# Performance work log

Hardware: AMD Instinct MI355X
Metric: run time of the kernel (lower is better)

## Reference

```python
import jax, jax.numpy as jnp
import numpy as np
from jax import lax

B, T, IN, H = 128, 1024, 256, 256


def setup_inputs() -> dict:
    key = jax.random.key(0)
    k1, k2, k3, k4 = jax.random.split(key, 4)
    return {
        "fullx": jax.random.normal(k1, (B, T, IN), dtype=jnp.float32),
        "h": jnp.zeros((B, H), dtype=jnp.float32),
        "c": jnp.zeros((B, H), dtype=jnp.float32),
        "wx": jax.random.normal(k2, (IN, 4 * H), dtype=jnp.float32) / (IN ** 0.5),
        "wh": jax.random.normal(k3, (H, 4 * H), dtype=jnp.float32) / (H ** 0.5),
        "b": jax.random.uniform(k4, (1, 4 * H), dtype=jnp.float32),
    }


def reference(fullx, h, c, wx, wh, b):
    hnum = h.shape[1]

    def step(carry, x_t):
        h, c = carry
        t = x_t @ wx + h @ wh + b  # [B, 4H]
        gate = jax.nn.sigmoid(t[:, : 3 * hnum])
        f = gate[:, :hnum]
        i = gate[:, hnum : 2 * hnum]
        o = gate[:, 2 * hnum : 3 * hnum]
        g = jnp.tanh(t[:, 3 * hnum : 4 * hnum])
        c_new = c * f + g * i
        h_new = jnp.tanh(c_new) * o
        return (h_new, c_new), h_new

    xs = jnp.swapaxes(fullx, 0, 1)  # [T, B, IN]
    (h_f, c_f), hs = lax.scan(step, (h, c), xs)
    fullh = jnp.swapaxes(hs, 0, 1)  # [B, T, H]
    return (fullh, h_f, c_f)
```

## Files before the change

kernel.cpp:

```cpp
#include <hip/hip_runtime.h>
#include <hip/hip_fp16.h>
#include <stdint.h>

#define Tdim 1024
#define INdim 256
#define Hdim 256
#define COLS 1024
#define NSLICE 8
#define NGRP 8
#define GB 16
#define UPB 32
#define CPB 128
#define NTHREADS 512
#define FLAG_STRIDE ((Tdim + 1) * NSLICE)
#define FLAG_BYTES (NGRP * FLAG_STRIDE * 4)
#define HBUF_OFF 266240

typedef _Float16 half8 __attribute__((ext_vector_type(8)));
typedef float f32x4 __attribute__((ext_vector_type(4)));

__device__ __forceinline__ uint16_t f2h(float f) {
    __half h = __float2half(f);
    return *reinterpret_cast<uint16_t*>(&h);
}
__device__ __forceinline__ float sigm(float v) {
    return __builtin_amdgcn_rcpf(1.f + __expf(-v));
}
__device__ __forceinline__ float tanhfast(float v) {
    float e = __expf(2.f * v);
    return 1.f - 2.f * __builtin_amdgcn_rcpf(e + 1.f);
}
__device__ __forceinline__ size_t hb_idx(int par, int grp, int m, int u) {
    return ((((size_t)par * NGRP + grp) * GB + m) << 8) | (size_t)u;
}

__global__ __launch_bounds__(NTHREADS, 1) void lstm_main(
    const float* __restrict__ x, const float* __restrict__ h0,
    const float* __restrict__ c0, const float* __restrict__ wx,
    const float* __restrict__ wh, const float* __restrict__ bias,
    float* __restrict__ out, uint32_t* flags, uint16_t* hbuf)
{
    const int tid   = threadIdx.x;
    const int grp   = blockIdx.x & 7;
    const int slice = blockIdx.x >> 3;
    const int lane  = tid & 63;
    const int wave  = tid >> 6;
    const int cw    = lane & 15;
    const int lhi   = lane >> 4;
    const int cl    = wave * 16 + cw;
    const int g     = cl & 3;
    const int ul    = cl >> 2;
    const int u     = slice * UPB + ul;
    const int gcol  = g * Hdim + u;

    __shared__ __align__(16) uint16_t Wl[CPB * 512];
    __shared__ __align__(16) uint16_t X[2][32][GB][8];
    __shared__ __align__(16) uint16_t Hs[32][GB][8];
    __shared__ __align__(16) uint16_t Hp16[GB][UPB];
    __shared__ __align__(16) float    Hpf[GB][UPB];

    for (int idx = tid; idx < CPB * 512; idx += NTHREADS) {
        int k  = idx >> 7;
        int ci = idx & 127;
        int uu = ci & 31, gg = ci >> 5;
        int cg = gg * Hdim + slice * UPB + uu;
        int c  = (uu << 2) | gg;
        float w = (k < INdim) ? wx[(size_t)k * COLS + cg]
                              : wh[(size_t)(k - INdim) * COLS + cg];
        int e = c * 512 + ((((k >> 3) ^ (c & 7)) << 3) | (k & 7));
        Wl[e] = f2h(w);
    }
    const int m_s  = tid >> 5;
    const int ko_s = tid & 31;
    {
        const float4* xs = reinterpret_cast<const float4*>(
            &x[((size_t)(grp * GB + m_s) * Tdim + 0) * INdim + ko_s * 8]);
        float4 a = xs[0], b = xs[1];
        uint16_t* xd = &X[0][ko_s][m_s][0];
        xd[0]=f2h(a.x); xd[1]=f2h(a.y); xd[2]=f2h(a.z); xd[3]=f2h(a.w);
        xd[4]=f2h(b.x); xd[5]=f2h(b.y); xd[6]=f2h(b.z); xd[7]=f2h(b.w);
    }
    float4 xp0, xp1;
    {
        const float4* xs = reinterpret_cast<const float4*>(
            &x[((size_t)(grp * GB + m_s) * Tdim + 1) * INdim + ko_s * 8]);
        xp0 = xs[0]; xp1 = xs[1];
    }
    if (tid < 64) {
        int m = tid >> 2, uo = tid & 3;
        int u0 = slice * UPB + uo * 8;
        const float4* hs = reinterpret_cast<const float4*>(
            &h0[(size_t)(grp * GB + m) * Hdim + u0]);
        float4 a = hs[0], b = hs[1];
        unsigned long long p0, p1;
        uint16_t* q0 = reinterpret_cast<uint16_t*>(&p0);
        uint16_t* q1 = reinterpret_cast<uint16_t*>(&p1);
        q0[0]=f2h(a.x); q0[1]=f2h(a.y); q0[2]=f2h(a.z); q0[3]=f2h(a.w);
        q1[0]=f2h(b.x); q1[1]=f2h(b.y); q1[2]=f2h(b.z); q1[3]=f2h(b.w);
        unsigned long long* hp =
            reinterpret_cast<unsigned long long*>(&hbuf[hb_idx(0, grp, m, u0)]);
        __hip_atomic_store(&hp[0], p0, __ATOMIC_RELAXED, __HIP_MEMORY_SCOPE_AGENT);
        __hip_atomic_store(&hp[1], p1, __ATOMIC_RELAXED, __HIP_MEMORY_SCOPE_AGENT);
    }
    float c_reg[4];
    #pragma unroll
    for (int r = 0; r < 4; ++r)
        c_reg[r] = c0[(size_t)(grp * GB + lhi * 4 + r) * Hdim + u];
    const float bv = bias[gcol];
    __syncthreads();
    uint32_t* fl = flags + grp * FLAG_STRIDE;
    if (tid == 0)
        __hip_atomic_store(&fl[slice], 1u, __ATOMIC_RELAXED, __HIP_MEMORY_SCOPE_AGENT);

    const uint32_t swz = (uint32_t)(cl & 7);
    const uint16_t* wrow = &Wl[cl * 512];
    float hv[4] = {0.f, 0.f, 0.f, 0.f};

    for (int t = 0; t < Tdim; ++t) {
        const int par = t & 1, pn = par ^ 1;

        {
            uint16_t* xd = &X[pn][ko_s][m_s][0];
            xd[0]=f2h(xp0.x); xd[1]=f2h(xp0.y); xd[2]=f2h(xp0.z); xd[3]=f2h(xp0.w);
            xd[4]=f2h(xp1.x); xd[5]=f2h(xp1.y); xd[6]=f2h(xp1.z); xd[7]=f2h(xp1.w);
        }
        {
            int tn = (t + 2 < Tdim) ? t + 2 : Tdim - 1;
            const float4* xs = reinterpret_cast<const float4*>(
                &x[((size_t)(grp * GB + m_s) * Tdim + tn) * INdim + ko_s * 8]);
            xp0 = xs[0]; xp1 = xs[1];
        }

        f32x4 acc0 = {0.f, 0.f, 0.f, 0.f}, acc1 = {0.f, 0.f, 0.f, 0.f};
        #pragma unroll
        for (int s = 0; s < 8; s += 2) {
            int ko0 = s * 4 + lhi, ko1 = ko0 + 4;
            half8 a0 = *reinterpret_cast<const half8*>(&X[par][ko0][cw][0]);
            half8 b0 = *reinterpret_cast<const half8*>(&wrow[(ko0 ^ swz) << 3]);
            acc0 = __builtin_amdgcn_mfma_f32_16x16x32_f16(a0, b0, acc0, 0, 0, 0);
            half8 a1 = *reinterpret_cast<const half8*>(&X[par][ko1][cw][0]);
            half8 b1 = *reinterpret_cast<const half8*>(&wrow[(ko1 ^ swz) << 3]);
            acc1 = __builtin_amdgcn_mfma_f32_16x16x32_f16(a1, b1, acc1, 0, 0, 0);
        }

        if (tid < NSLICE) {
            while (__hip_atomic_load(&fl[t * NSLICE + tid], __ATOMIC_RELAXED,
                                     __HIP_MEMORY_SCOPE_AGENT) == 0) {}
        }
        __syncthreads();

        {
            const unsigned long long* hp = reinterpret_cast<const unsigned long long*>(
                &hbuf[hb_idx(par, grp, m_s, ko_s * 8)]);
            unsigned long long h0v = __hip_atomic_load(&hp[0], __ATOMIC_RELAXED,
                                                       __HIP_MEMORY_SCOPE_AGENT);
            unsigned long long h1v = __hip_atomic_load(&hp[1], __ATOMIC_RELAXED,
                                                       __HIP_MEMORY_SCOPE_AGENT);
            *reinterpret_cast<unsigned long long*>(&Hs[ko_s][m_s][0]) = h0v;
            *reinterpret_cast<unsigned long long*>(&Hs[ko_s][m_s][4]) = h1v;
        }
        __syncthreads();

        #pragma unroll
        for (int s = 0; s < 8; s += 2) {
            int ko0 = s * 4 + lhi, ko1 = ko0 + 4;
            half8 a0 = *reinterpret_cast<const half8*>(&Hs[ko0][cw][0]);
            half8 b0 = *reinterpret_cast<const half8*>(&wrow[((32 + ko0) ^ swz) << 3]);
            acc0 = __builtin_amdgcn_mfma_f32_16x16x32_f16(a0, b0, acc0, 0, 0, 0);
            half8 a1 = *reinterpret_cast<const half8*>(&Hs[ko1][cw][0]);
            half8 b1 = *reinterpret_cast<const half8*>(&wrow[((32 + ko1) ^ swz) << 3]);
            acc1 = __builtin_amdgcn_mfma_f32_16x16x32_f16(a1, b1, acc1, 0, 0, 0);
        }

        #pragma unroll
        for (int r = 0; r < 4; ++r) {
            float tval = acc0[r] + acc1[r] + bv;
            float act = (g == 3) ? tanhfast(tval) : sigm(tval);
            float x1  = __shfl_xor(act, 1);
            float e0  = (g & 1) ? x1 : act;
            float o1  = (g & 1) ? act : x1;
            float e0s = __shfl_xor(e0, 2);
            float o1s = __shfl_xor(o1, 2);
            float f_ = (g < 2) ? e0  : e0s;
            float i_ = (g < 2) ? o1  : o1s;
            float o_ = (g < 2) ? e0s : e0;
            float g_ = (g < 2) ? o1s : o1;
            c_reg[r] = fmaf(c_reg[r], f_, g_ * i_);
            hv[r] = tanhfast(c_reg[r]) * o_;
        }

        if (g == 0) {
            #pragma unroll
            for (int r = 0; r < 4; ++r) {
                int m = lhi * 4 + r;
                Hp16[m][ul] = f2h(hv[r]);
                Hpf[m][ul]  = hv[r];
            }
        }
        __syncthreads();

        if (tid < 128) {
            int m = tid >> 3, q = tid & 7;
            unsigned long long v =
                *reinterpret_cast<const unsigned long long*>(&Hp16[m][q * 4]);
            __hip_atomic_store(reinterpret_cast<unsigned long long*>(
                                   &hbuf[hb_idx(pn, grp, m, slice * UPB + q * 4)]),
                               v, __ATOMIC_RELAXED, __HIP_MEMORY_SCOPE_AGENT);
        }
        __syncthreads();
        if (tid == 0)
            __hip_atomic_store(&fl[(t + 1) * NSLICE + slice], 1u,
                               __ATOMIC_RELAXED, __HIP_MEMORY_SCOPE_AGENT);

        if (tid >= 128 && tid < 256) {
            int j = tid - 128;
            int m = j >> 3, q = j & 7;
            float4 v = *reinterpret_cast<const float4*>(&Hpf[m][q * 4]);
            *reinterpret_cast<float4*>(
                &out[((size_t)(grp * GB + m) * Tdim + t) * Hdim + slice * UPB + q * 4]) = v;
        }
    }

    if (g == 0) {
        const size_t fsz = (size_t)(NGRP * GB) * Tdim * Hdim;
        #pragma unroll
        for (int r = 0; r < 4; ++r) {
            int m = lhi * 4 + r;
            out[fsz + (size_t)(grp * GB + m) * Hdim + u] = hv[r];
            out[fsz + (size_t)(NGRP * GB) * Hdim + (size_t)(grp * GB + m) * Hdim + u] = c_reg[r];
        }
    }
}

extern "C" void kernel_launch(void* const* d_in, const int* in_sizes, int n_in,
                              void* d_out, int out_size, void* d_ws, size_t ws_size,
                              hipStream_t stream) {
    const float* x    = (const float*)d_in[0];
    const float* h0   = (const float*)d_in[1];
    const float* c0   = (const float*)d_in[2];
    const float* wx   = (const float*)d_in[3];
    const float* wh   = (const float*)d_in[4];
    const float* bias = (const float*)d_in[5];
    float* out = (float*)d_out;
    uint32_t* flags = (uint32_t*)d_ws;
    uint16_t* hbuf  = (uint16_t*)((char*)d_ws + HBUF_OFF);

    hipMemsetAsync(flags, 0, FLAG_BYTES, stream);

    void* args[] = {(void*)&x, (void*)&h0, (void*)&c0, (void*)&wx, (void*)&wh,
                    (void*)&bias, (void*)&out, (void*)&flags, (void*)&hbuf};
    hipLaunchCooperativeKernel((const void*)lstm_main, dim3(NSLICE * NGRP),
                               dim3(NTHREADS), args, 0, stream);
}
```

Before: 2.601 ms.

## Keep weight fragments in registers and swizzle X/H shared layout

Each lane now loads its 16 weight fragments from LDS into registers once before the time loop, so the per-step MFMAs no longer read weights from shared memory. The X and H staging buffers are reordered to [m][k] with an XOR swizzle, which is meant to avoid bank conflicts. Stores into them are packed into single 16-byte writes instead of scalar half stores. This adds 64 VGPRs per lane to hold the weights, which is allowed since the kernel runs one 512-thread block per CU.

```diff
diff --git a/kernel.cpp b/kernel.cpp
--- a/kernel.cpp
+++ b/kernel.cpp
@@ -22,6 +22,9 @@
 __device__ __forceinline__ uint16_t f2h(float f) {
     __half h = __float2half(f);
     return *reinterpret_cast<uint16_t*>(&h);
+}
+__device__ __forceinline__ uint32_t pk2(float lo, float hi) {
+    return (uint32_t)f2h(lo) | ((uint32_t)f2h(hi) << 16);
 }
 __device__ __forceinline__ float sigm(float v) {
     return __builtin_amdgcn_rcpf(1.f + __expf(-v));
@@ -54,8 +57,8 @@
     const int gcol  = g * Hdim + u;
 
     __shared__ __align__(16) uint16_t Wl[CPB * 512];
-    __shared__ __align__(16) uint16_t X[2][32][GB][8];
-    __shared__ __align__(16) uint16_t Hs[32][GB][8];
+    __shared__ __align__(16) uint16_t X[2][GB][32][8];
+    __shared__ __align__(16) uint16_t Hs[GB][32][8];
     __shared__ __align__(16) uint16_t Hp16[GB][UPB];
     __shared__ __align__(16) float    Hpf[GB][UPB];
 
@@ -70,15 +73,15 @@
         int e = c * 512 + ((((k >> 3) ^ (c & 7)) << 3) | (k & 7));
         Wl[e] = f2h(w);
     }
-    const int m_s  = tid >> 5;
-    const int ko_s = tid & 31;
+    const int m_s   = tid >> 5;
+    const int ko_s  = tid & 31;
+    const int slt_s = ko_s ^ (m_s & 7);
     {
         const float4* xs = reinterpret_cast<const float4*>(
             &x[((size_t)(grp * GB + m_s) * Tdim + 0) * INdim + ko_s * 8]);
         float4 a = xs[0], b = xs[1];
-        uint16_t* xd = &X[0][ko_s][m_s][0];
-        xd[0]=f2h(a.x); xd[1]=f2h(a.y); xd[2]=f2h(a.z); xd[3]=f2h(a.w);
-        xd[4]=f2h(b.x); xd[5]=f2h(b.y); xd[6]=f2h(b.z); xd[7]=f2h(b.w);
+        uint4 pkv = {pk2(a.x, a.y), pk2(a.z, a.w), pk2(b.x, b.y), pk2(b.z, b.w)};
+        *reinterpret_cast<uint4*>(&X[0][m_s][slt_s][0]) = pkv;
     }
     float4 xp0, xp1;
     {
@@ -92,11 +95,10 @@
         const float4* hs = reinterpret_cast<const float4*>(
             &h0[(size_t)(grp * GB + m) * Hdim + u0]);
         float4 a = hs[0], b = hs[1];
-        unsigned long long p0, p1;
-        uint16_t* q0 = reinterpret_cast<uint16_t*>(&p0);
-        uint16_t* q1 = reinterpret_cast<uint16_t*>(&p1);
-        q0[0]=f2h(a.x); q0[1]=f2h(a.y); q0[2]=f2h(a.z); q0[3]=f2h(a.w);
-        q1[0]=f2h(b.x); q1[1]=f2h(b.y); q1[2]=f2h(b.z); q1[3]=f2h(b.w);
+        unsigned long long p0 =
+            (unsigned long long)pk2(a.x, a.y) | ((unsigned long long)pk2(a.z, a.w) << 32);
+        unsigned long long p1 =
+            (unsigned long long)pk2(b.x, b.y) | ((unsigned long long)pk2(b.z, b.w) << 32);
         unsigned long long* hp =
             reinterpret_cast<unsigned long long*>(&hbuf[hb_idx(0, grp, m, u0)]);
         __hip_atomic_store(&hp[0], p0, __ATOMIC_RELAXED, __HIP_MEMORY_SCOPE_AGENT);
@@ -114,15 +116,21 @@
 
     const uint32_t swz = (uint32_t)(cl & 7);
     const uint16_t* wrow = &Wl[cl * 512];
+    half8 Wf[16];
+    #pragma unroll
+    for (int i = 0; i < 16; ++i)
+        Wf[i] = *reinterpret_cast<const half8*>(&wrow[(((uint32_t)(i * 4 + lhi)) ^ swz) << 3]);
+
+    const int swz_a = cw & 7;
     float hv[4] = {0.f, 0.f, 0.f, 0.f};
 
     for (int t = 0; t < Tdim; ++t) {
         const int par = t & 1, pn = par ^ 1;
 
         {
-            uint16_t* xd = &X[pn][ko_s][m_s][0];
-            xd[0]=f2h(xp0.x); xd[1]=f2h(xp0.y); xd[2]=f2h(xp0.z); xd[3]=f2h(xp0.w);
-            xd[4]=f2h(xp1.x); xd[5]=f2h(xp1.y); xd[6]=f2h(xp1.z); xd[7]=f2h(xp1.w);
+            uint4 pkv = {pk2(xp0.x, xp0.y), pk2(xp0.z, xp0.w),
+                         pk2(xp1.x, xp1.y), pk2(xp1.z, xp1.w)};
+            *reinterpret_cast<uint4*>(&X[pn][m_s][slt_s][0]) = pkv;
         }
         {
             int tn = (t + 2 < Tdim) ? t + 2 : Tdim - 1;
@@ -135,12 +143,10 @@
         #pragma unroll
         for (int s = 0; s < 8; s += 2) {
             int ko0 = s * 4 + lhi, ko1 = ko0 + 4;
-            half8 a0 = *reinterpret_cast<const half8*>(&X[par][ko0][cw][0]);
-            half8 b0 = *reinterpret_cast<const half8*>(&wrow[(ko0 ^ swz) << 3]);
-            acc0 = __builtin_amdgcn_mfma_f32_16x16x32_f16(a0, b0, acc0, 0, 0, 0);
-            half8 a1 = *reinterpret_cast<const half8*>(&X[par][ko1][cw][0]);
-            half8 b1 = *reinterpret_cast<const half8*>(&wrow[(ko1 ^ swz) << 3]);
-            acc1 = __builtin_amdgcn_mfma_f32_16x16x32_f16(a1, b1, acc1, 0, 0, 0);
+            half8 a0 = *reinterpret_cast<const half8*>(&X[par][cw][ko0 ^ swz_a][0]);
+            acc0 = __builtin_amdgcn_mfma_f32_16x16x32_f16(a0, Wf[s], acc0, 0, 0, 0);
+            half8 a1 = *reinterpret_cast<const half8*>(&X[par][cw][ko1 ^ swz_a][0]);
+            acc1 = __builtin_amdgcn_mfma_f32_16x16x32_f16(a1, Wf[s + 1], acc1, 0, 0, 0);
         }
 
         if (tid < NSLICE) {
@@ -156,20 +162,19 @@
                                                        __HIP_MEMORY_SCOPE_AGENT);
             unsigned long long h1v = __hip_atomic_load(&hp[1], __ATOMIC_RELAXED,
                                                        __HIP_MEMORY_SCOPE_AGENT);
-            *reinterpret_cast<unsigned long long*>(&Hs[ko_s][m_s][0]) = h0v;
-            *reinterpret_cast<unsigned long long*>(&Hs[ko_s][m_s][4]) = h1v;
+            uint4 hw = {(uint32_t)h0v, (uint32_t)(h0v >> 32),
+                        (uint32_t)h1v, (uint32_t)(h1v >> 32)};
+            *reinterpret_cast<uint4*>(&Hs[m_s][slt_s][0]) = hw;
         }
         __syncthreads();
 
         #pragma unroll
         for (int s = 0; s < 8; s += 2) {
             int ko0 = s * 4 + lhi, ko1 = ko0 + 4;
-            half8 a0 = *reinterpret_cast<const half8*>(&Hs[ko0][cw][0]);
-            half8 b0 = *reinterpret_cast<const half8*>(&wrow[((32 + ko0) ^ swz) << 3]);
-            acc0 = __builtin_amdgcn_mfma_f32_16x16x32_f16(a0, b0, acc0, 0, 0, 0);
-            half8 a1 = *reinterpret_cast<const half8*>(&Hs[ko1][cw][0]);
-            half8 b1 = *reinterpret_cast<const half8*>(&wrow[((32 + ko1) ^ swz) << 3]);
-            acc1 = __builtin_amdgcn_mfma_f32_16x16x32_f16(a1, b1, acc1, 0, 0, 0);
+            half8 a0 = *reinterpret_cast<const half8*>(&Hs[cw][ko0 ^ swz_a][0]);
+            acc0 = __builtin_amdgcn_mfma_f32_16x16x32_f16(a0, Wf[8 + s], acc0, 0, 0, 0);
+            half8 a1 = *reinterpret_cast<const half8*>(&Hs[cw][ko1 ^ swz_a][0]);
+            acc1 = __builtin_amdgcn_mfma_f32_16x16x32_f16(a1, Wf[9 + s], acc1, 0, 0, 0);
         }
 
         #pragma unroll
```

Measured after the change: 2.308 ms. 11.2% less time.
